# Kernel tuning notes

Hardware: AMD Instinct MI355X
Metric: run time of the kernel (lower is better)

## Reference

```python
import jax, jax.numpy as jnp
import numpy as np

K = 20
EPS = 1e-5
SLOPE = 0.2


def lrelu(z):
    return jnp.where(z >= 0, z, SLOPE * z)


def knn(x, k):
    # x: [B, C, N] -> idx of k nearest neighbors [B, N, K]
    inner = -2.0 * jnp.einsum('bcn,bcm->bnm', x, x)
    xx = jnp.sum(x * x, axis=1)  # [B, N]
    pd = -xx[:, :, None] - inner - xx[:, None, :]  # negative squared distance
    _, idx = jax.lax.top_k(pd, k)
    return idx


def graph_feature(x, k):
    # x: [B, C, N] -> [B, 2C, N, K] = cat(neighbor - center, center)
    B, C, N = x.shape
    idx = knn(x, k)                                  # [B, N, K]
    x_bnc = jnp.transpose(x, (0, 2, 1))              # [B, N, C]
    nbr = x_bnc[jnp.arange(B)[:, None, None], idx]   # [B, N, K, C]
    ctr = x_bnc[:, :, None, :]                       # [B, N, 1, C]
    feat = jnp.concatenate(
        [nbr - ctr, jnp.broadcast_to(ctr, nbr.shape)], axis=-1)  # [B, N, K, 2C]
    return jnp.transpose(feat, (0, 3, 1, 2))         # [B, 2C, N, K]


def conv_bn_lrelu(x, w, g, b):
    # 1x1 conv (no bias) + BatchNorm2d (batch stats, train mode) + LeakyReLU(0.2)
    y = jnp.einsum('oc,bcnk->bonk', w, x)
    m = y.mean(axis=(0, 2, 3), keepdims=True)
    v = y.var(axis=(0, 2, 3), keepdims=True)
    y = (y - m) / jnp.sqrt(v + EPS) * g.reshape(1, -1, 1, 1) + b.reshape(1, -1, 1, 1)
    return lrelu(y)


def setup_inputs() -> dict:
    key = jax.random.key(0)
    ks = jax.random.split(key, 10)
    f32 = jnp.float32
    d = {
        'x': jax.random.normal(ks[0], (1, 3, 8, 4096), dtype=f32),
        'conv1_w': jax.random.normal(ks[1], (16, 6), dtype=f32) * 0.2,
        'bn1_g': jnp.ones((16,), f32), 'bn1_b': jnp.zeros((16,), f32),
        'conv2_w': jax.random.normal(ks[2], (32, 38), dtype=f32) * 0.1,
        'bn2_g': jnp.ones((32,), f32), 'bn2_b': jnp.zeros((32,), f32),
        'convd1_w': jax.random.normal(ks[3], (32, 32), dtype=f32) * 0.1,
        'bnd1_g': jnp.ones((32,), f32), 'bnd1_b': jnp.zeros((32,), f32),
        'convd2_w': jax.random.normal(ks[4], (32, 64), dtype=f32) * 0.1,
        'bnd2_g': jnp.ones((32,), f32), 'bnd2_b': jnp.zeros((32,), f32),
        'l1_w': jax.random.normal(ks[5], (64, 64), dtype=f32) * 0.1,
        'l1_b': jnp.zeros((64,), f32),
        'l2_w': jax.random.normal(ks[6], (32, 64), dtype=f32) * 0.1,
        'l2_b': jnp.zeros((32,), f32),
        'l3_w': jax.random.normal(ks[7], (11, 32), dtype=f32) * 0.1,
        'l3_b': jnp.zeros((11,), f32),
    }
    return d


def reference(x, conv1_w, bn1_g, bn1_b, conv2_w, bn2_g, bn2_b,
              convd1_w, bnd1_g, bnd1_b, convd2_w, bnd2_g, bnd2_b,
              l1_w, l1_b, l2_w, l2_b, l3_w, l3_b):
    x = jnp.transpose(x[0], (1, 0, 2))  # [B, 3, N]
    B, _, N = x.shape
    x1_gf = graph_feature(x, K)                                   # [B, 6, N, K]
    x1_max = conv_bn_lrelu(x1_gf, conv1_w, bn1_g, bn1_b).max(-1)  # [B, 16, N]
    gf16 = graph_feature(x1_max, K)                               # [B, 32, N, K]
    x2_gf = jnp.concatenate([x1_gf, gf16], axis=1)                # [B, 38, N, K]
    x2_max = conv_bn_lrelu(x2_gf, conv2_w, bn2_g, bn2_b).max(-1)  # [B, 32, N]
    xd1 = conv_bn_lrelu(gf16, convd1_w, bnd1_g, bnd1_b).max(-1)   # [B, 32, N]
    xd2 = conv_bn_lrelu(graph_feature(x2_max, K),
                        convd2_w, bnd2_g, bnd2_b).max(-1)          # [B, 32, N]
    h = jnp.concatenate([xd1, xd2], axis=1)                        # [B, 64, N]
    h = h.reshape(B, -1, 64).mean(axis=1)                          # raw view, as in torch
    h = lrelu(h @ l1_w.T + l1_b)
    h = lrelu(h @ l2_w.T + l2_b)
    return lrelu(h @ l3_w.T + l3_b)                                # [B, 11]
```

## Files before the change

kernel.cpp:

```cpp
#include <hip/hip_runtime.h>
#include <cstddef>

#define DI __device__ __forceinline__

constexpr int NB  = 8;
constexpr int NP  = 4096;
constexpr int KNN = 20;

DI float lrelu(float z) { return z >= 0.f ? z : 0.2f * z; }

__global__ void k_prep(const float* __restrict__ xin, float* __restrict__ xt,
                       float* __restrict__ xx) {
  int t = blockIdx.x * blockDim.x + threadIdx.x;
  int b = t >> 12, n = t & (NP - 1);
  float c0 = xin[(0 * NB + b) * NP + n];
  float c1 = xin[(1 * NB + b) * NP + n];
  float c2 = xin[(2 * NB + b) * NP + n];
  *reinterpret_cast<float4*>(xt + (size_t)t * 4) = make_float4(c0, c1, c2, 0.f);
  xx[t] = c0 * c0 + c1 * c1 + c2 * c2;
}

template<int C>
__global__ void k_xx(const float* __restrict__ X, float* __restrict__ xx) {
  int bn = blockIdx.x * blockDim.x + threadIdx.x;
  float s = 0.f;
#pragma unroll
  for (int c = 0; c < C; c += 4) {
    float4 a = *reinterpret_cast<const float4*>(X + (size_t)bn * C + c);
    s += a.x * a.x + a.y * a.y + a.z * a.z + a.w * a.w;
  }
  xx[bn] = s;
}

template<int C, int P>
__global__ __launch_bounds__(256) void k_knn(const float* __restrict__ Xq,
                                             const float* __restrict__ XT,
                                             const float* __restrict__ xx,
                                             int* __restrict__ idxout) {
  constexpr int CH = NP / P;
  constexpr int SL = P / 64;
  constexpr int F4 = C / 4;
  constexpr int LD = P * F4 / 256;
  __shared__ float4 lds4[2 * P * F4];

  int wv   = threadIdx.x >> 6;
  int lane = threadIdx.x & 63;
  int row  = blockIdx.x * 4 + wv;
  int b = row >> 12, n = row & (NP - 1);
  const float*  Xqb  = Xq + (size_t)b * NP * C;
  const float4* srcT = reinterpret_cast<const float4*>(XT + (size_t)b * NP * C);
  const float*  xxb  = xx + (size_t)b * NP;

  float q[C];
#pragma unroll
  for (int c = 0; c < C; c += 4) {
    float4 a = *reinterpret_cast<const float4*>(Xqb + (size_t)n * C + c);
    q[c] = a.x; q[c + 1] = a.y; q[c + 2] = a.z; q[c + 3] = a.w;
  }
  float xxn = xxb[n];

  float v[64];
  float gv[4]; int gj[4];
#pragma unroll
  for (int g = 0; g < 4; ++g) { gv[g] = -3.0e38f; gj[g] = 0; }

  float4 nxt[LD];
#pragma unroll
  for (int i = 0; i < LD; ++i) {
    int u = i * 256 + (int)threadIdx.x;
    nxt[i] = srcT[(size_t)(u / P) * NP + (u % P)];
  }

#pragma unroll
  for (int ch = 0; ch < CH; ++ch) {
    float4* B = lds4 + (ch & 1) * (P * F4);
#pragma unroll
    for (int i = 0; i < LD; ++i)
      B[i * 256 + (int)threadIdx.x] = nxt[i];
    __syncthreads();
    if (ch + 1 < CH) {
#pragma unroll
      for (int i = 0; i < LD; ++i) {
        int u = i * 256 + (int)threadIdx.x;
        nxt[i] = srcT[(size_t)(u / P) * NP + (size_t)(ch + 1) * P + (u % P)];
      }
    }
#pragma unroll
    for (int sl = 0; sl < SL; ++sl) {
      const int s = ch * SL + sl;
      int p = sl * 64 + lane;
      float xxm = xxb[s * 64 + lane];
      float dp[4] = {0.f, 0.f, 0.f, 0.f};
#pragma unroll
      for (int cg = 0; cg < F4; ++cg) {
        float4 a = B[cg * P + p];
        dp[cg & 3] = fmaf(q[cg * 4 + 0], a.x, dp[cg & 3]);
        dp[cg & 3] = fmaf(q[cg * 4 + 1], a.y, dp[cg & 3]);
        dp[cg & 3] = fmaf(q[cg * 4 + 2], a.z, dp[cg & 3]);
        dp[cg & 3] = fmaf(q[cg * 4 + 3], a.w, dp[cg & 3]);
      }
      float dot = (dp[0] + dp[1]) + (dp[2] + dp[3]);
      float val = 2.f * dot - xxm - xxn;
      v[s] = val;
      const int g = s >> 4;
      bool better = val > gv[g];
      gv[g] = better ? val : gv[g];
      gj[g] = better ? s   : gj[g];
    }
  }

  int gi[4];
#pragma unroll
  for (int g = 0; g < 4; ++g) gi[g] = (gj[g] << 6) | lane;

  int myidx = 0;
#pragma unroll 1
  for (int t = 0; t < KNN; ++t) {
    float bv = gv[0]; int bi = gi[0];
#pragma unroll
    for (int g = 1; g < 4; ++g) {
      bool bet = gv[g] > bv;
      bv = bet ? gv[g] : bv;
      bi = bet ? gi[g] : bi;
    }
#pragma unroll
    for (int off = 32; off >= 1; off >>= 1) {
      float ov = __shfl_xor(bv, off);
      int   oi = __shfl_xor(bi, off);
      bool bet = (ov > bv) || (ov == bv && oi < bi);
      bv = bet ? ov : bv;
      bi = bet ? oi : bi;
    }
    if (lane == t) myidx = bi;
    if (lane == (bi & 63)) {
      int jw = bi >> 6;
      int g  = jw >> 4;
#pragma unroll
      for (int G = 0; G < 4; ++G) {
        if (g == G) {
          float nv = -3.0e38f; int nj = 0;
#pragma unroll
          for (int jj = G * 16; jj < G * 16 + 16; ++jj) {
            v[jj] = (jj == jw) ? -3.4e38f : v[jj];
            bool bet = v[jj] > nv;
            nv = bet ? v[jj] : nv;
            nj = bet ? jj : nj;
          }
          gv[G] = nv;
          gi[G] = (nj << 6) | lane;
        }
      }
    }
  }
  if (lane < KNN) idxout[(size_t)row * KNN + lane] = myidx;
}

template<int CG>
DI void block_reduce_write(float (&s)[CG], float (&ss)[CG], float* red, float* out) {
#pragma unroll
  for (int o = 0; o < CG; ++o) {
#pragma unroll
    for (int off = 32; off >= 1; off >>= 1) {
      s[o]  += __shfl_xor(s[o],  off);
      ss[o] += __shfl_xor(ss[o], off);
    }
  }
  int lane = threadIdx.x & 63, wv = threadIdx.x >> 6;
  if (lane == 0) {
#pragma unroll
    for (int o = 0; o < CG; ++o) {
      red[wv * 2 * CG + o]      = s[o];
      red[wv * 2 * CG + CG + o] = ss[o];
    }
  }
  __syncthreads();
  if ((int)threadIdx.x < 2 * CG) {
    out[threadIdx.x] = red[0 * 2 * CG + threadIdx.x] + red[1 * 2 * CG + threadIdx.x] +
                       red[2 * 2 * CG + threadIdx.x] + red[3 * 2 * CG + threadIdx.x];
  }
}

template<int COUT, int CG, int OG, int KG>
__global__ void k_bnfin(const float* __restrict__ parts, const float* __restrict__ g,
                        const float* __restrict__ bb, float* __restrict__ bnp) {
  constexpr int G = 256 / COUT;
  __shared__ float red[512];
  int tid = threadIdx.x;
  int sub = tid / COUT, o = tid % COUT;
  int og = o / CG, oo = o % CG;
  float S = 0.f, SS = 0.f;
  for (int z = 0; z < KG; ++z)
    for (int x = sub; x < 128; x += G) {
      size_t p = ((size_t)(z * OG + og) * 128 + x) * (2 * CG);
      S  += parts[p + oo];
      SS += parts[p + CG + oo];
    }
  red[tid] = S; red[256 + tid] = SS;
  __syncthreads();
  if (tid < COUT) {
    S = 0.f; SS = 0.f;
#pragma unroll
    for (int gg = 0; gg < G; ++gg) { S += red[gg * COUT + tid]; SS += red[256 + gg * COUT + tid]; }
    const float cnt = (float)NB * NP * KNN;
    float m   = S / cnt;
    float var = SS / cnt - m * m;
    float sc  = g[tid] / sqrtf(var + 1e-5f);
    bnp[tid]        = sc;
    bnp[COUT + tid] = bb[tid] - m * sc;
  }
}

__global__ __launch_bounds__(256) void k_stats1(const float* __restrict__ xt,
    const int* __restrict__ idx1, const float* __restrict__ w, float* __restrict__ parts) {
  __shared__ float red[4 * 32];
  int bn = blockIdx.x * 256 + threadIdx.x;
  int b = bn >> 12;
  float4 ctr = *reinterpret_cast<const float4*>(xt + (size_t)bn * 4);
  float base[16], s[16], ss[16];
#pragma unroll
  for (int o = 0; o < 16; ++o) {
    const float* wo = w + o * 6;
    base[o] = (wo[3] - wo[0]) * ctr.x + (wo[4] - wo[1]) * ctr.y + (wo[5] - wo[2]) * ctr.z;
    s[o] = 0.f; ss[o] = 0.f;
  }
  const int* ip = idx1 + (size_t)bn * KNN + blockIdx.z * 10;
  for (int kk = 0; kk < 10; ++kk) {
    int m = ip[kk];
    float4 nb = *reinterpret_cast<const float4*>(xt + (size_t)(b * NP + m) * 4);
#pragma unroll
    for (int o = 0; o < 16; ++o) {
      const float* wo = w + o * 6;
      float y = fmaf(wo[0], nb.x, fmaf(wo[1], nb.y, fmaf(wo[2], nb.z, base[o])));
      s[o] += y; ss[o] = fmaf(y, y, ss[o]);
    }
  }
  size_t p = ((size_t)blockIdx.z * 128 + blockIdx.x) * 32;
  block_reduce_write<16>(s, ss, red, parts + p);
}

__global__ __launch_bounds__(256) void k_apply1(const float* __restrict__ xt,
    const int* __restrict__ idx1, const float* __restrict__ w, const float* __restrict__ bnp,
    float* __restrict__ x1m, float* __restrict__ x1mT) {
  int bn = blockIdx.x * 256 + threadIdx.x;
  int og = blockIdx.y * 8;
  int b = bn >> 12, pidx = bn & (NP - 1);
  float4 ctr = *reinterpret_cast<const float4*>(xt + (size_t)bn * 4);
  float base[8], mx[8];
#pragma unroll
  for (int o = 0; o < 8; ++o) {
    const float* wo = w + (og + o) * 6;
    base[o] = (wo[3] - wo[0]) * ctr.x + (wo[4] - wo[1]) * ctr.y + (wo[5] - wo[2]) * ctr.z;
    mx[o] = -3.0e38f;
  }
  const int* ip = idx1 + (size_t)bn * KNN;
  for (int k = 0; k < KNN; ++k) {
    int m = ip[k];
    float4 nb = *reinterpret_cast<const float4*>(xt + (size_t)(b * NP + m) * 4);
#pragma unroll
    for (int o = 0; o < 8; ++o) {
      const float* wo = w + (og + o) * 6;
      float y = fmaf(wo[0], nb.x, fmaf(wo[1], nb.y, fmaf(wo[2], nb.z, base[o])));
      mx[o] = fmaxf(mx[o], lrelu(y * bnp[og + o] + bnp[16 + og + o]));
    }
  }
#pragma unroll
  for (int o = 0; o < 8; ++o) x1m[(size_t)bn * 16 + og + o] = mx[o];
  int cg0 = og >> 2;
  float4 lo = make_float4(mx[0], mx[1], mx[2], mx[3]);
  float4 hi = make_float4(mx[4], mx[5], mx[6], mx[7]);
  reinterpret_cast<float4*>(x1mT)[(size_t)b * NP * 4 + (size_t)cg0 * NP + pidx] = lo;
  reinterpret_cast<float4*>(x1mT)[(size_t)b * NP * 4 + (size_t)(cg0 + 1) * NP + pidx] = hi;
}

__global__ __launch_bounds__(256) void k_stats2(const float* __restrict__ xt,
    const float* __restrict__ x1m, const int* __restrict__ idx1, const int* __restrict__ idx2,
    const float* __restrict__ w, float* __restrict__ parts) {
  __shared__ float red[4 * 16];
  int bn = blockIdx.x * 256 + threadIdx.x;
  int og = blockIdx.y * 8;
  int b = bn >> 12;
  float4 ctr3 = *reinterpret_cast<const float4*>(xt + (size_t)bn * 4);
  float base[8], s[8], ss[8];
#pragma unroll
  for (int o = 0; o < 8; ++o) {
    const float* wo = w + (og + o) * 38;
    base[o] = (wo[3] - wo[0]) * ctr3.x + (wo[4] - wo[1]) * ctr3.y + (wo[5] - wo[2]) * ctr3.z;
    s[o] = 0.f; ss[o] = 0.f;
  }
#pragma unroll
  for (int cg = 0; cg < 4; ++cg) {
    float4 a = *reinterpret_cast<const float4*>(x1m + (size_t)bn * 16 + cg * 4);
#pragma unroll
    for (int o = 0; o < 8; ++o) {
      const float* wo = w + (og + o) * 38;
      base[o] += (wo[22 + cg*4] - wo[6 + cg*4]) * a.x + (wo[23 + cg*4] - wo[7 + cg*4]) * a.y +
                 (wo[24 + cg*4] - wo[8 + cg*4]) * a.z + (wo[25 + cg*4] - wo[9 + cg*4]) * a.w;
    }
  }
  const int* i1 = idx1 + (size_t)bn * KNN + blockIdx.z * 10;
  const int* i2 = idx2 + (size_t)bn * KNN + blockIdx.z * 10;
  for (int kk = 0; kk < 10; ++kk) {
    int m1 = i1[kk], m2 = i2[kk];
    float4 nb3 = *reinterpret_cast<const float4*>(xt + (size_t)(b * NP + m1) * 4);
    float4 a0 = *reinterpret_cast<const float4*>(x1m + (size_t)(b * NP + m2) * 16 + 0);
    float4 a1 = *reinterpret_cast<const float4*>(x1m + (size_t)(b * NP + m2) * 16 + 4);
    float4 a2 = *reinterpret_cast<const float4*>(x1m + (size_t)(b * NP + m2) * 16 + 8);
    float4 a3 = *reinterpret_cast<const float4*>(x1m + (size_t)(b * NP + m2) * 16 + 12);
#pragma unroll
    for (int o = 0; o < 8; ++o) {
      const float* wo = w + (og + o) * 38;
      float y = base[o];
      y = fmaf(wo[0], nb3.x, y); y = fmaf(wo[1], nb3.y, y); y = fmaf(wo[2], nb3.z, y);
      y = fmaf(wo[6],  a0.x, y); y = fmaf(wo[7],  a0.y, y); y = fmaf(wo[8],  a0.z, y); y = fmaf(wo[9],  a0.w, y);
      y = fmaf(wo[10], a1.x, y); y = fmaf(wo[11], a1.y, y); y = fmaf(wo[12], a1.z, y); y = fmaf(wo[13], a1.w, y);
      y = fmaf(wo[14], a2.x, y); y = fmaf(wo[15], a2.y, y); y = fmaf(wo[16], a2.z, y); y = fmaf(wo[17], a2.w, y);
      y = fmaf(wo[18], a3.x, y); y = fmaf(wo[19], a3.y, y); y = fmaf(wo[20], a3.z, y); y = fmaf(wo[21], a3.w, y);
      s[o] += y; ss[o] = fmaf(y, y, ss[o]);
    }
  }
  size_t p = ((size_t)(blockIdx.z * 4 + blockIdx.y) * 128 + blockIdx.x) * 16;
  block_reduce_write<8>(s, ss, red, parts + p);
}

__global__ __launch_bounds__(256) void k_apply2(const float* __restrict__ xt,
    const float* __restrict__ x1m, const int* __restrict__ idx1, const int* __restrict__ idx2,
    const float* __restrict__ w, const float* __restrict__ bnp, float* __restrict__ x2m,
    float* __restrict__ x2mT) {
  int bn = blockIdx.x * 256 + threadIdx.x;
  int og = blockIdx.y * 8;
  int b = bn >> 12, pidx = bn & (NP - 1);
  float4 ctr3 = *reinterpret_cast<const float4*>(xt + (size_t)bn * 4);
  float base[8], mx[8];
#pragma unroll
  for (int o = 0; o < 8; ++o) {
    const float* wo = w + (og + o) * 38;
    base[o] = (wo[3] - wo[0]) * ctr3.x + (wo[4] - wo[1]) * ctr3.y + (wo[5] - wo[2]) * ctr3.z;
    mx[o] = -3.0e38f;
  }
#pragma unroll
  for (int cg = 0; cg < 4; ++cg) {
    float4 a = *reinterpret_cast<const float4*>(x1m + (size_t)bn * 16 + cg * 4);
#pragma unroll
    for (int o = 0; o < 8; ++o) {
      const float* wo = w + (og + o) * 38;
      base[o] += (wo[22 + cg*4] - wo[6 + cg*4]) * a.x + (wo[23 + cg*4] - wo[7 + cg*4]) * a.y +
                 (wo[24 + cg*4] - wo[8 + cg*4]) * a.z + (wo[25 + cg*4] - wo[9 + cg*4]) * a.w;
    }
  }
  const int* i1 = idx1 + (size_t)bn * KNN;
  const int* i2 = idx2 + (size_t)bn * KNN;
  for (int k = 0; k < KNN; ++k) {
    int m1 = i1[k], m2 = i2[k];
    float4 nb3 = *reinterpret_cast<const float4*>(xt + (size_t)(b * NP + m1) * 4);
    float4 a0 = *reinterpret_cast<const float4*>(x1m + (size_t)(b * NP + m2) * 16 + 0);
    float4 a1 = *reinterpret_cast<const float4*>(x1m + (size_t)(b * NP + m2) * 16 + 4);
    float4 a2 = *reinterpret_cast<const float4*>(x1m + (size_t)(b * NP + m2) * 16 + 8);
    float4 a3 = *reinterpret_cast<const float4*>(x1m + (size_t)(b * NP + m2) * 16 + 12);
#pragma unroll
    for (int o = 0; o < 8; ++o) {
      const float* wo = w + (og + o) * 38;
      float y = base[o];
      y = fmaf(wo[0], nb3.x, y); y = fmaf(wo[1], nb3.y, y); y = fmaf(wo[2], nb3.z, y);
      y = fmaf(wo[6],  a0.x, y); y = fmaf(wo[7],  a0.y, y); y = fmaf(wo[8],  a0.z, y); y = fmaf(wo[9],  a0.w, y);
      y = fmaf(wo[10], a1.x, y); y = fmaf(wo[11], a1.y, y); y = fmaf(wo[12], a1.z, y); y = fmaf(wo[13], a1.w, y);
      y = fmaf(wo[14], a2.x, y); y = fmaf(wo[15], a2.y, y); y = fmaf(wo[16], a2.z, y); y = fmaf(wo[17], a2.w, y);
      y = fmaf(wo[18], a3.x, y); y = fmaf(wo[19], a3.y, y); y = fmaf(wo[20], a3.z, y); y = fmaf(wo[21], a3.w, y);
      mx[o] = fmaxf(mx[o], lrelu(y * bnp[og + o] + bnp[32 + og + o]));
    }
  }
#pragma unroll
  for (int o = 0; o < 8; ++o) x2m[(size_t)bn * 32 + og + o] = mx[o];
  int cg0 = og >> 2;
  float4 lo = make_float4(mx[0], mx[1], mx[2], mx[3]);
  float4 hi = make_float4(mx[4], mx[5], mx[6], mx[7]);
  reinterpret_cast<float4*>(x2mT)[(size_t)b * NP * 8 + (size_t)cg0 * NP + pidx] = lo;
  reinterpret_cast<float4*>(x2mT)[(size_t)b * NP * 8 + (size_t)(cg0 + 1) * NP + pidx] = hi;
}

__global__ __launch_bounds__(256) void k_statsd1(const float* __restrict__ x1m,
    const int* __restrict__ idx2, const float* __restrict__ w, float* __restrict__ parts) {
  __shared__ float red[4 * 16];
  int bn = blockIdx.x * 256 + threadIdx.x;
  int og = blockIdx.y * 8;
  int b = bn >> 12;
  float base[8], s[8], ss[8];
#pragma unroll
  for (int o = 0; o < 8; ++o) { base[o] = 0.f; s[o] = 0.f; ss[o] = 0.f; }
#pragma unroll
  for (int cg = 0; cg < 4; ++cg) {
    float4 a = *reinterpret_cast<const float4*>(x1m + (size_t)bn * 16 + cg * 4);
#pragma unroll
    for (int o = 0; o < 8; ++o) {
      const float* wo = w + (og + o) * 32;
      base[o] += (wo[16 + cg*4] - wo[cg*4]) * a.x + (wo[17 + cg*4] - wo[1 + cg*4]) * a.y +
                 (wo[18 + cg*4] - wo[2 + cg*4]) * a.z + (wo[19 + cg*4] - wo[3 + cg*4]) * a.w;
    }
  }
  const int* i2 = idx2 + (size_t)bn * KNN + blockIdx.z * 10;
  for (int kk = 0; kk < 10; ++kk) {
    int m2 = i2[kk];
    float4 a0 = *reinterpret_cast<const float4*>(x1m + (size_t)(b * NP + m2) * 16 + 0);
    float4 a1 = *reinterpret_cast<const float4*>(x1m + (size_t)(b * NP + m2) * 16 + 4);
    float4 a2 = *reinterpret_cast<const float4*>(x1m + (size_t)(b * NP + m2) * 16 + 8);
    float4 a3 = *reinterpret_cast<const float4*>(x1m + (size_t)(b * NP + m2) * 16 + 12);
#pragma unroll
    for (int o = 0; o < 8; ++o) {
      const float* wo = w + (og + o) * 32;
      float y = base[o];
      y = fmaf(wo[0],  a0.x, y); y = fmaf(wo[1],  a0.y, y); y = fmaf(wo[2],  a0.z, y); y = fmaf(wo[3],  a0.w, y);
      y = fmaf(wo[4],  a1.x, y); y = fmaf(wo[5],  a1.y, y); y = fmaf(wo[6],  a1.z, y); y = fmaf(wo[7],  a1.w, y);
      y = fmaf(wo[8],  a2.x, y); y = fmaf(wo[9],  a2.y, y); y = fmaf(wo[10], a2.z, y); y = fmaf(wo[11], a2.w, y);
      y = fmaf(wo[12], a3.x, y); y = fmaf(wo[13], a3.y, y); y = fmaf(wo[14], a3.z, y); y = fmaf(wo[15], a3.w, y);
      s[o] += y; ss[o] = fmaf(y, y, ss[o]);
    }
  }
  size_t p = ((size_t)(blockIdx.z * 4 + blockIdx.y) * 128 + blockIdx.x) * 16;
  block_reduce_write<8>(s, ss, red, parts + p);
}

__global__ __launch_bounds__(256) void k_applyd1(const float* __restrict__ x1m,
    const int* __restrict__ idx2, const float* __restrict__ w, const float* __restrict__ bnp,
    float* __restrict__ xd1) {
  int bn = blockIdx.x * 256 + threadIdx.x;
  int og = blockIdx.y * 8;
  int b = bn >> 12;
  float base[8], mx[8];
#pragma unroll
  for (int o = 0; o < 8; ++o) { base[o] = 0.f; mx[o] = -3.0e38f; }
#pragma unroll
  for (int cg = 0; cg < 4; ++cg) {
    float4 a = *reinterpret_cast<const float4*>(x1m + (size_t)bn * 16 + cg * 4);
#pragma unroll
    for (int o = 0; o < 8; ++o) {
      const float* wo = w + (og + o) * 32;
      base[o] += (wo[16 + cg*4] - wo[cg*4]) * a.x + (wo[17 + cg*4] - wo[1 + cg*4]) * a.y +
                 (wo[18 + cg*4] - wo[2 + cg*4]) * a.z + (wo[19 + cg*4] - wo[3 + cg*4]) * a.w;
    }
  }
  const int* i2 = idx2 + (size_t)bn * KNN;
  for (int k = 0; k < KNN; ++k) {
    int m2 = i2[k];
    float4 a0 = *reinterpret_cast<const float4*>(x1m + (size_t)(b * NP + m2) * 16 + 0);
    float4 a1 = *reinterpret_cast<const float4*>(x1m + (size_t)(b * NP + m2) * 16 + 4);
    float4 a2 = *reinterpret_cast<const float4*>(x1m + (size_t)(b * NP + m2) * 16 + 8);
    float4 a3 = *reinterpret_cast<const float4*>(x1m + (size_t)(b * NP + m2) * 16 + 12);
#pragma unroll
    for (int o = 0; o < 8; ++o) {
      const float* wo = w + (og + o) * 32;
      float y = base[o];
      y = fmaf(wo[0],  a0.x, y); y = fmaf(wo[1],  a0.y, y); y = fmaf(wo[2],  a0.z, y); y = fmaf(wo[3],  a0.w, y);
      y = fmaf(wo[4],  a1.x, y); y = fmaf(wo[5],  a1.y, y); y = fmaf(wo[6],  a1.z, y); y = fmaf(wo[7],  a1.w, y);
      y = fmaf(wo[8],  a2.x, y); y = fmaf(wo[9],  a2.y, y); y = fmaf(wo[10], a2.z, y); y = fmaf(wo[11], a2.w, y);
      y = fmaf(wo[12], a3.x, y); y = fmaf(wo[13], a3.y, y); y = fmaf(wo[14], a3.z, y); y = fmaf(wo[15], a3.w, y);
      mx[o] = fmaxf(mx[o], lrelu(y * bnp[og + o] + bnp[32 + og + o]));
    }
  }
#pragma unroll
  for (int o = 0; o < 8; ++o) xd1[(size_t)bn * 32 + og + o] = mx[o];
}

__global__ __launch_bounds__(256) void k_statsd2(const float* __restrict__ x2m,
    const int* __restrict__ idx3, const float* __restrict__ w, float* __restrict__ parts) {
  __shared__ float red[4 * 16];
  int bn = blockIdx.x * 256 + threadIdx.x;
  int og = blockIdx.y * 8;
  int b = bn >> 12;
  float base[8], s[8], ss[8];
#pragma unroll
  for (int o = 0; o < 8; ++o) { base[o] = 0.f; s[o] = 0.f; ss[o] = 0.f; }
#pragma unroll
  for (int cg = 0; cg < 8; ++cg) {
    float4 a = *reinterpret_cast<const float4*>(x2m + (size_t)bn * 32 + cg * 4);
#pragma unroll
    for (int o = 0; o < 8; ++o) {
      const float* wo = w + (og + o) * 64;
      base[o] += (wo[32 + cg*4] - wo[cg*4]) * a.x + (wo[33 + cg*4] - wo[1 + cg*4]) * a.y +
                 (wo[34 + cg*4] - wo[2 + cg*4]) * a.z + (wo[35 + cg*4] - wo[3 + cg*4]) * a.w;
    }
  }
  const int* i3 = idx3 + (size_t)bn * KNN + blockIdx.z * 10;
  for (int kk = 0; kk < 10; ++kk) {
    int m3 = i3[kk];
    const float* np = x2m + (size_t)(b * NP + m3) * 32;
    float4 a0 = *reinterpret_cast<const float4*>(np + 0);
    float4 a1 = *reinterpret_cast<const float4*>(np + 4);
    float4 a2 = *reinterpret_cast<const float4*>(np + 8);
    float4 a3 = *reinterpret_cast<const float4*>(np + 12);
    float4 a4 = *reinterpret_cast<const float4*>(np + 16);
    float4 a5 = *reinterpret_cast<const float4*>(np + 20);
    float4 a6 = *reinterpret_cast<const float4*>(np + 24);
    float4 a7 = *reinterpret_cast<const float4*>(np + 28);
#pragma unroll
    for (int o = 0; o < 8; ++o) {
      const float* wo = w + (og + o) * 64;
      float y = base[o];
      y = fmaf(wo[0],  a0.x, y); y = fmaf(wo[1],  a0.y, y); y = fmaf(wo[2],  a0.z, y); y = fmaf(wo[3],  a0.w, y);
      y = fmaf(wo[4],  a1.x, y); y = fmaf(wo[5],  a1.y, y); y = fmaf(wo[6],  a1.z, y); y = fmaf(wo[7],  a1.w, y);
      y = fmaf(wo[8],  a2.x, y); y = fmaf(wo[9],  a2.y, y); y = fmaf(wo[10], a2.z, y); y = fmaf(wo[11], a2.w, y);
      y = fmaf(wo[12], a3.x, y); y = fmaf(wo[13], a3.y, y); y = fmaf(wo[14], a3.z, y); y = fmaf(wo[15], a3.w, y);
      y = fmaf(wo[16], a4.x, y); y = fmaf(wo[17], a4.y, y); y = fmaf(wo[18], a4.z, y); y = fmaf(wo[19], a4.w, y);
      y = fmaf(wo[20], a5.x, y); y = fmaf(wo[21], a5.y, y); y = fmaf(wo[22], a5.z, y); y = fmaf(wo[23], a5.w, y);
      y = fmaf(wo[24], a6.x, y); y = fmaf(wo[25], a6.y, y); y = fmaf(wo[26], a6.z, y); y = fmaf(wo[27], a6.w, y);
      y = fmaf(wo[28], a7.x, y); y = fmaf(wo[29], a7.y, y); y = fmaf(wo[30], a7.z, y); y = fmaf(wo[31], a7.w, y);
      s[o] += y; ss[o] = fmaf(y, y, ss[o]);
    }
  }
  size_t p = ((size_t)(blockIdx.z * 4 + blockIdx.y) * 128 + blockIdx.x) * 16;
  block_reduce_write<8>(s, ss, red, parts + p);
}

__global__ __launch_bounds__(256) void k_applyd2(const float* __restrict__ x2m,
    const int* __restrict__ idx3, const float* __restrict__ w, const float* __restrict__ bnp,
    float* __restrict__ xd2) {
  int bn = blockIdx.x * 256 + threadIdx.x;
  int og = blockIdx.y * 8;
  int b = bn >> 12;
  float base[8], mx[8];
#pragma unroll
  for (int o = 0; o < 8; ++o) { base[o] = 0.f; mx[o] = -3.0e38f; }
#pragma unroll
  for (int cg = 0; cg < 8; ++cg) {
    float4 a = *reinterpret_cast<const float4*>(x2m + (size_t)bn * 32 + cg * 4);
#pragma unroll
    for (int o = 0; o < 8; ++o) {
      const float* wo = w + (og + o) * 64;
      base[o] += (wo[32 + cg*4] - wo[cg*4]) * a.x + (wo[33 + cg*4] - wo[1 + cg*4]) * a.y +
                 (wo[34 + cg*4] - wo[2 + cg*4]) * a.z + (wo[35 + cg*4] - wo[3 + cg*4]) * a.w;
    }
  }
  const int* i3 = idx3 + (size_t)bn * KNN;
  for (int k = 0; k < KNN; ++k) {
    int m3 = i3[k];
    const float* np = x2m + (size_t)(b * NP + m3) * 32;
    float4 a0 = *reinterpret_cast<const float4*>(np + 0);
    float4 a1 = *reinterpret_cast<const float4*>(np + 4);
    float4 a2 = *reinterpret_cast<const float4*>(np + 8);
    float4 a3 = *reinterpret_cast<const float4*>(np + 12);
    float4 a4 = *reinterpret_cast<const float4*>(np + 16);
    float4 a5 = *reinterpret_cast<const float4*>(np + 20);
    float4 a6 = *reinterpret_cast<const float4*>(np + 24);
    float4 a7 = *reinterpret_cast<const float4*>(np + 28);
#pragma unroll
    for (int o = 0; o < 8; ++o) {
      const float* wo = w + (og + o) * 64;
      float y = base[o];
      y = fmaf(wo[0],  a0.x, y); y = fmaf(wo[1],  a0.y, y); y = fmaf(wo[2],  a0.z, y); y = fmaf(wo[3],  a0.w, y);
      y = fmaf(wo[4],  a1.x, y); y = fmaf(wo[5],  a1.y, y); y = fmaf(wo[6],  a1.z, y); y = fmaf(wo[7],  a1.w, y);
      y = fmaf(wo[8],  a2.x, y); y = fmaf(wo[9],  a2.y, y); y = fmaf(wo[10], a2.z, y); y = fmaf(wo[11], a2.w, y);
      y = fmaf(wo[12], a3.x, y); y = fmaf(wo[13], a3.y, y); y = fmaf(wo[14], a3.z, y); y = fmaf(wo[15], a3.w, y);
      y = fmaf(wo[16], a4.x, y); y = fmaf(wo[17], a4.y, y); y = fmaf(wo[18], a4.z, y); y = fmaf(wo[19], a4.w, y);
      y = fmaf(wo[20], a5.x, y); y = fmaf(wo[21], a5.y, y); y = fmaf(wo[22], a5.z, y); y = fmaf(wo[23], a5.w, y);
      y = fmaf(wo[24], a6.x, y); y = fmaf(wo[25], a6.y, y); y = fmaf(wo[26], a6.z, y); y = fmaf(wo[27], a6.w, y);
      y = fmaf(wo[28], a7.x, y); y = fmaf(wo[29], a7.y, y); y = fmaf(wo[30], a7.z, y); y = fmaf(wo[31], a7.w, y);
      mx[o] = fmaxf(mx[o], lrelu(y * bnp[og + o] + bnp[32 + og + o]));
    }
  }
#pragma unroll
  for (int o = 0; o < 8; ++o) xd2[(size_t)bn * 32 + og + o] = mx[o];
}

__global__ void k_mean(const float* __restrict__ xd1, const float* __restrict__ xd2,
                       float* __restrict__ hm) {
  int b = blockIdx.x >> 6, j = blockIdx.x & 63;
  int tt = threadIdx.x;
  const float* p1 = xd1 + ((size_t)(b * NP) + tt * 64 + j) * 32;
  const float* p2 = xd2 + ((size_t)(b * NP) + tt * 64 + j) * 32;
  float s = 0.f;
#pragma unroll
  for (int c = 0; c < 32; c += 4) {
    float4 a = *reinterpret_cast<const float4*>(p1 + c);
    s += a.x + a.y + a.z + a.w;
  }
#pragma unroll
  for (int c = 0; c < 32; c += 4) {
    float4 a = *reinterpret_cast<const float4*>(p2 + c);
    s += a.x + a.y + a.z + a.w;
  }
#pragma unroll
  for (int off = 32; off >= 1; off >>= 1) s += __shfl_xor(s, off);
  if (tt == 0) hm[blockIdx.x] = s * (1.f / 4096.f);
}

__global__ void k_mlp(const float* __restrict__ hm,
                      const float* __restrict__ w1, const float* __restrict__ b1,
                      const float* __restrict__ w2, const float* __restrict__ b2,
                      const float* __restrict__ w3, const float* __restrict__ b3,
                      float* __restrict__ out) {
  __shared__ float h0[512], h1[512], h2[256];
  int t = threadIdx.x;
  h0[t] = hm[t];
  __syncthreads();
  {
    int b = t >> 6, o = t & 63;
    float a = b1[o];
    for (int j = 0; j < 64; ++j) a += h0[b * 64 + j] * w1[o * 64 + j];
    h1[t] = lrelu(a);
  }
  __syncthreads();
  if (t < 256) {
    int b = t >> 5, o = t & 31;
    float a = b2[o];
    for (int j = 0; j < 64; ++j) a += h1[b * 64 + j] * w2[o * 64 + j];
    h2[t] = lrelu(a);
  }
  __syncthreads();
  if (t < 88) {
    int b = t / 11, o = t % 11;
    float a = b3[o];
    for (int j = 0; j < 32; ++j) a += h2[b * 32 + j] * w3[o * 32 + j];
    out[t] = lrelu(a);
  }
}

extern "C" void kernel_launch(void* const* d_in, const int* in_sizes, int n_in,
                              void* d_out, int out_size, void* d_ws, size_t ws_size,
                              hipStream_t stream) {
  const float* xin = (const float*)d_in[0];
  const float* w1  = (const float*)d_in[1];
  const float* g1  = (const float*)d_in[2];
  const float* bb1 = (const float*)d_in[3];
  const float* w2  = (const float*)d_in[4];
  const float* g2  = (const float*)d_in[5];
  const float* bb2 = (const float*)d_in[6];
  const float* wd1 = (const float*)d_in[7];
  const float* gd1 = (const float*)d_in[8];
  const float* bbd1= (const float*)d_in[9];
  const float* wd2 = (const float*)d_in[10];
  const float* gd2 = (const float*)d_in[11];
  const float* bbd2= (const float*)d_in[12];
  const float* l1w = (const float*)d_in[13];
  const float* l1b = (const float*)d_in[14];
  const float* l2w = (const float*)d_in[15];
  const float* l2b = (const float*)d_in[16];
  const float* l3w = (const float*)d_in[17];
  const float* l3b = (const float*)d_in[18];
  float* out = (float*)d_out;

  float* W = (float*)d_ws;
  float* xt    = W;
  float* xx1   = W + 131072;
  float* xx2   = W + 163840;
  float* xx3   = W + 196608;
  float* x1m   = W + 229376;
  float* x2m   = W + 753664;
  float* xd1   = W + 1802240;
  float* xd2   = W + 2850816;
  float* hmean = W + 3899392;
  float* bnp1  = W + 3899904;
  float* bnp2  = W + 3899968;
  float* bnpd1 = W + 3900032;
  float* bnpd2 = W + 3900096;
  float* parts = W + 3900160;
  int* idx1 = (int*)(W + 3932928);
  int* idx2 = idx1 + 655360;
  int* idx3 = idx2 + 655360;
  float* x1mT = xd1;
  float* x2mT = xd2;

  k_prep<<<128, 256, 0, stream>>>(xin, xt, xx1);
  k_knn<4, 1024><<<8192, 256, 0, stream>>>(xt, xt, xx1, idx1);

  k_stats1<<<dim3(128, 1, 2), 256, 0, stream>>>(xt, idx1, w1, parts);
  k_bnfin<16, 16, 1, 2><<<1, 256, 0, stream>>>(parts, g1, bb1, bnp1);
  k_apply1<<<dim3(128, 2), 256, 0, stream>>>(xt, idx1, w1, bnp1, x1m, x1mT);
  k_xx<16><<<128, 256, 0, stream>>>(x1m, xx2);
  k_knn<16, 256><<<8192, 256, 0, stream>>>(x1m, x1mT, xx2, idx2);

  k_stats2<<<dim3(128, 4, 2), 256, 0, stream>>>(xt, x1m, idx1, idx2, w2, parts);
  k_bnfin<32, 8, 4, 2><<<1, 256, 0, stream>>>(parts, g2, bb2, bnp2);
  k_apply2<<<dim3(128, 4), 256, 0, stream>>>(xt, x1m, idx1, idx2, w2, bnp2, x2m, x2mT);
  k_xx<32><<<128, 256, 0, stream>>>(x2m, xx3);

  k_statsd1<<<dim3(128, 4, 2), 256, 0, stream>>>(x1m, idx2, wd1, parts);
  k_bnfin<32, 8, 4, 2><<<1, 256, 0, stream>>>(parts, gd1, bbd1, bnpd1);
  k_applyd1<<<dim3(128, 4), 256, 0, stream>>>(x1m, idx2, wd1, bnpd1, xd1);

  k_knn<32, 128><<<8192, 256, 0, stream>>>(x2m, x2mT, xx3, idx3);
  k_statsd2<<<dim3(128, 4, 2), 256, 0, stream>>>(x2m, idx3, wd2, parts);
  k_bnfin<32, 8, 4, 2><<<1, 256, 0, stream>>>(parts, gd2, bbd2, bnpd2);
  k_applyd2<<<dim3(128, 4), 256, 0, stream>>>(x2m, idx3, wd2, bnpd2, xd2);

  k_mean<<<512, 64, 0, stream>>>(xd1, xd2, hmean);
  k_mlp<<<1, 512, 0, stream>>>(hmean, l1w, l1b, l2w, l2b, l3w, l3b, out);
}
```

Measured before the change: 1.563 ms.

## Split kNN candidate scan across two wavefronts per query and merge top-k

For the 16- and 32-channel kNN passes, each query row is now handled by two wavefronts. Each wavefront scans alternating LDS chunks of candidates, keeping a 32-slot register buffer instead of 64, and computes a partial top-20. The two partial lists are merged by rank counting through shared memory. Launching twice as many blocks raises parallelism and lowers per-thread register pressure. In exchange, each block loads the same candidate tiles while computing only half as many rows, so global-to-LDS traffic per query doubles, and the merge adds a block-wide sync.

```diff
diff --git a/kernel.cpp b/kernel.cpp
--- a/kernel.cpp
+++ b/kernel.cpp
@@ -32,7 +32,7 @@
   xx[bn] = s;
 }
 
-template<int C, int P>
+template<int C, int P, bool HALF>
 __global__ __launch_bounds__(256) void k_knn(const float* __restrict__ Xq,
                                              const float* __restrict__ XT,
                                              const float* __restrict__ xx,
@@ -41,11 +41,17 @@
   constexpr int SL = P / 64;
   constexpr int F4 = C / 4;
   constexpr int LD = P * F4 / 256;
+  constexpr int NSLOT = HALF ? 32 : 64;
+  constexpr int NG = NSLOT / 16;
   __shared__ float4 lds4[2 * P * F4];
+  __shared__ float mv[4][20];
+  __shared__ int   mi[4][20];
 
   int wv   = threadIdx.x >> 6;
   int lane = threadIdx.x & 63;
-  int row  = blockIdx.x * 4 + wv;
+  int r, h, row;
+  if (HALF) { r = wv >> 1; h = wv & 1; row = blockIdx.x * 2 + r; }
+  else      { r = wv;      h = 0;      row = blockIdx.x * 4 + wv; }
   int b = row >> 12, n = row & (NP - 1);
   const float*  Xqb  = Xq + (size_t)b * NP * C;
   const float4* srcT = reinterpret_cast<const float4*>(XT + (size_t)b * NP * C);
@@ -59,10 +65,10 @@
   }
   float xxn = xxb[n];
 
-  float v[64];
-  float gv[4]; int gj[4];
-#pragma unroll
-  for (int g = 0; g < 4; ++g) { gv[g] = -3.0e38f; gj[g] = 0; }
+  float v[NSLOT];
+  float gv[NG]; int gj[NG];
+#pragma unroll
+  for (int g = 0; g < NG; ++g) { gv[g] = -3.0e38f; gj[g] = 0; }
 
   float4 nxt[LD];
 #pragma unroll
@@ -85,43 +91,43 @@
         nxt[i] = srcT[(size_t)(u / P) * NP + (size_t)(ch + 1) * P + (u % P)];
       }
     }
-#pragma unroll
-    for (int sl = 0; sl < SL; ++sl) {
-      const int s = ch * SL + sl;
-      int p = sl * 64 + lane;
-      float xxm = xxb[s * 64 + lane];
-      float dp[4] = {0.f, 0.f, 0.f, 0.f};
-#pragma unroll
-      for (int cg = 0; cg < F4; ++cg) {
-        float4 a = B[cg * P + p];
-        dp[cg & 3] = fmaf(q[cg * 4 + 0], a.x, dp[cg & 3]);
-        dp[cg & 3] = fmaf(q[cg * 4 + 1], a.y, dp[cg & 3]);
-        dp[cg & 3] = fmaf(q[cg * 4 + 2], a.z, dp[cg & 3]);
-        dp[cg & 3] = fmaf(q[cg * 4 + 3], a.w, dp[cg & 3]);
+    if (!HALF || ((ch & 1) == h)) {
+#pragma unroll
+      for (int sl = 0; sl < SL; ++sl) {
+        const int sg   = ch * SL + sl;
+        const int lidx = HALF ? ((ch >> 1) * SL + sl) : sg;
+        int p = sl * 64 + lane;
+        int cand = sg * 64 + lane;
+        float xxm = xxb[cand];
+        float dp[4] = {0.f, 0.f, 0.f, 0.f};
+#pragma unroll
+        for (int cg = 0; cg < F4; ++cg) {
+          float4 a = B[cg * P + p];
+          dp[cg & 3] = fmaf(q[cg * 4 + 0], a.x, dp[cg & 3]);
+          dp[cg & 3] = fmaf(q[cg * 4 + 1], a.y, dp[cg & 3]);
+          dp[cg & 3] = fmaf(q[cg * 4 + 2], a.z, dp[cg & 3]);
+          dp[cg & 3] = fmaf(q[cg * 4 + 3], a.w, dp[cg & 3]);
+        }
+        float dot = (dp[0] + dp[1]) + (dp[2] + dp[3]);
+        float val = 2.f * dot - xxm - xxn;
+        v[lidx] = val;
+        const int g = lidx >> 4;
+        bool better = val > gv[g];
+        gv[g] = better ? val  : gv[g];
+        gj[g] = better ? cand : gj[g];
       }
-      float dot = (dp[0] + dp[1]) + (dp[2] + dp[3]);
-      float val = 2.f * dot - xxm - xxn;
-      v[s] = val;
-      const int g = s >> 4;
-      bool better = val > gv[g];
-      gv[g] = better ? val : gv[g];
-      gj[g] = better ? s   : gj[g];
-    }
-  }
-
-  int gi[4];
-#pragma unroll
-  for (int g = 0; g < 4; ++g) gi[g] = (gj[g] << 6) | lane;
-
-  int myidx = 0;
+    }
+  }
+
+  float myv = -3.0e38f; int myi = 0;
 #pragma unroll 1
   for (int t = 0; t < KNN; ++t) {
-    float bv = gv[0]; int bi = gi[0];
-#pragma unroll
-    for (int g = 1; g < 4; ++g) {
+    float bv = gv[0]; int bi = gj[0];
+#pragma unroll
+    for (int g = 1; g < NG; ++g) {
       bool bet = gv[g] > bv;
       bv = bet ? gv[g] : bv;
-      bi = bet ? gi[g] : bi;
+      bi = bet ? gj[g] : bi;
     }
 #pragma unroll
     for (int off = 32; off >= 1; off >>= 1) {
@@ -131,28 +137,50 @@
       bv = bet ? ov : bv;
       bi = bet ? oi : bi;
     }
-    if (lane == t) myidx = bi;
+    if (lane == t) { myv = bv; myi = bi; }
     if (lane == (bi & 63)) {
-      int jw = bi >> 6;
-      int g  = jw >> 4;
-#pragma unroll
-      for (int G = 0; G < 4; ++G) {
+      int lg = bi >> 6;
+      int lw = HALF ? (((lg / SL) >> 1) * SL + (lg % SL)) : lg;
+      int g  = lw >> 4;
+#pragma unroll
+      for (int G = 0; G < NG; ++G) {
         if (g == G) {
           float nv = -3.0e38f; int nj = 0;
 #pragma unroll
           for (int jj = G * 16; jj < G * 16 + 16; ++jj) {
-            v[jj] = (jj == jw) ? -3.4e38f : v[jj];
+            v[jj] = (jj == lw) ? -3.4e38f : v[jj];
             bool bet = v[jj] > nv;
             nv = bet ? v[jj] : nv;
             nj = bet ? jj : nj;
           }
           gv[G] = nv;
-          gi[G] = (nj << 6) | lane;
+          int sg = HALF ? (((nj / SL) * 2 + h) * SL + (nj % SL)) : nj;
+          gj[G] = (sg << 6) | lane;
         }
       }
     }
   }
-  if (lane < KNN) idxout[(size_t)row * KNN + lane] = myidx;
+
+  if (!HALF) {
+    if (lane < KNN) idxout[(size_t)row * KNN + lane] = myi;
+  } else {
+    if (lane < KNN) { mv[wv][lane] = myv; mi[wv][lane] = myi; }
+    __syncthreads();
+    if (wv < 2) {
+      const float* fv = &mv[wv * 2][0];
+      const int*   fi = &mi[wv * 2][0];
+      float ev = (lane < 40) ? fv[lane] : -3.4e38f;
+      int   ei = (lane < 40) ? fi[lane] : -1;
+      int rk = 0;
+#pragma unroll 4
+      for (int j = 0; j < 40; ++j) {
+        float jv = fv[j]; int ji = fi[j];
+        rk += ((jv > ev) || (jv == ev && ji < ei)) ? 1 : 0;
+      }
+      int orow = blockIdx.x * 2 + wv;
+      if (lane < 40 && rk < KNN) idxout[(size_t)orow * KNN + rk] = ei;
+    }
+  }
 }
 
 template<int CG>
@@ -658,13 +686,13 @@
   float* x2mT = xd2;
 
   k_prep<<<128, 256, 0, stream>>>(xin, xt, xx1);
-  k_knn<4, 1024><<<8192, 256, 0, stream>>>(xt, xt, xx1, idx1);
+  k_knn<4, 1024, false><<<8192, 256, 0, stream>>>(xt, xt, xx1, idx1);
 
   k_stats1<<<dim3(128, 1, 2), 256, 0, stream>>>(xt, idx1, w1, parts);
   k_bnfin<16, 16, 1, 2><<<1, 256, 0, stream>>>(parts, g1, bb1, bnp1);
   k_apply1<<<dim3(128, 2), 256, 0, stream>>>(xt, idx1, w1, bnp1, x1m, x1mT);
   k_xx<16><<<128, 256, 0, stream>>>(x1m, xx2);
-  k_knn<16, 256><<<8192, 256, 0, stream>>>(x1m, x1mT, xx2, idx2);
+  k_knn<16, 256, true><<<16384, 256, 0, stream>>>(x1m, x1mT, xx2, idx2);
 
   k_stats2<<<dim3(128, 4, 2), 256, 0, stream>>>(xt, x1m, idx1, idx2, w2, parts);
   k_bnfin<32, 8, 4, 2><<<1, 256, 0, stream>>>(parts, g2, bb2, bnp2);
@@ -675,7 +703,7 @@
   k_bnfin<32, 8, 4, 2><<<1, 256, 0, stream>>>(parts, gd1, bbd1, bnpd1);
   k_applyd1<<<dim3(128, 4), 256, 0, stream>>>(x1m, idx2, wd1, bnpd1, xd1);
 
-  k_knn<32, 128><<<8192, 256, 0, stream>>>(x2m, x2mT, xx3, idx3);
+  k_knn<32, 128, true><<<16384, 256, 0, stream>>>(x2m, x2mT, xx3, idx3);
   k_statsd2<<<dim3(128, 4, 2), 256, 0, stream>>>(x2m, idx3, wd2, parts);
   k_bnfin<32, 8, 4, 2><<<1, 256, 0, stream>>>(parts, gd2, bbd2, bnpd2);
   k_applyd2<<<dim3(128, 4), 256, 0, stream>>>(x2m, idx3, wd2, bnpd2, xd2);
```

Result: slower. 2.109 ms (+34.9%).
